# Kernel optimization log

Hardware: AMD Instinct MI355X
Metric: run time of the kernel (lower is better)

## Reference

```python
import jax, jax.numpy as jnp
import numpy as np

N_NODES = 100000
N_EDGES = 3200000
C, H, F = 512, 256, 64


def spmm(edge_row, edge_col, edge_val, Z):
    # (A @ Z)[i] = sum over edges e with row[e]==i of val[e] * Z[col[e]]
    msgs = edge_val[:, None] * Z[edge_col]  # [E, d]
    return jax.ops.segment_sum(msgs, edge_row, num_segments=N_NODES)


def setup_inputs() -> dict:
    key = jax.random.key(0)
    k1, k2, k3, k4, k5, k6, k7 = jax.random.split(key, 7)
    X = jax.random.normal(k1, (N_NODES, C), dtype=jnp.float32)
    edge_row = jax.random.randint(k2, (N_EDGES,), 0, N_NODES, dtype=jnp.int32)
    edge_col = jax.random.randint(k3, (N_EDGES,), 0, N_NODES, dtype=jnp.int32)
    edge_val = jax.random.uniform(k4, (N_EDGES,), dtype=jnp.float32)
    W0 = jax.random.normal(k5, (C, H), dtype=jnp.float32) * (C ** -0.5)
    Wh1 = jax.random.normal(k6, (H, H), dtype=jnp.float32) * (H ** -0.5)
    W1 = jax.random.normal(k7, (H, F), dtype=jnp.float32) * (H ** -0.5)
    return {"X": X, "edge_row": edge_row, "edge_col": edge_col,
            "edge_val": edge_val, "W0": W0, "Wh1": Wh1, "W1": W1}


def reference(X, edge_row, edge_col, edge_val, W0, Wh1, W1):
    # layer 0: relu(A @ (X W0))   (dropout=0 -> identity)
    Z = jax.nn.relu(spmm(edge_row, edge_col, edge_val, X @ W0))
    # hidden layers (num_layers - 2 = 1)
    Z = jax.nn.relu(spmm(edge_row, edge_col, edge_val, Z @ Wh1))
    # output layer: softmax(A @ (Z W1), axis=-1)
    Z = jax.nn.softmax(spmm(edge_row, edge_col, edge_val, Z @ W1), axis=-1)
    return Z
```

## Files before the change

### kernel.cpp

```cpp
#include <hip/hip_runtime.h>
#include <cstdint>
#include <cstddef>


#define SCAN_B 1024

typedef __attribute__((ext_vector_type(8))) short short8_t;
typedef __attribute__((ext_vector_type(4))) short short4_t;
typedef __attribute__((ext_vector_type(4))) float f32x4;

__device__ __forceinline__ short bf16_hi(float x) {
    union { float f; unsigned u; } c; c.f = x;
    return (short)(c.u >> 16);
}
__device__ __forceinline__ float bf16_f32(short h) {
    union { float f; unsigned u; } c; c.u = ((unsigned)(unsigned short)h) << 16;
    return c.f;
}

__device__ __forceinline__ void gload_lds16(const void* g, void* l) {
    __builtin_amdgcn_global_load_lds(
        (const __attribute__((address_space(1))) void*)g,
        (__attribute__((address_space(3))) void*)l, 16, 0, 0);
}

#define GBAR() asm volatile("s_barrier" ::: "memory")
#define LGKM0() asm volatile("s_waitcnt lgkmcnt(0)" ::: "memory")

__device__ __forceinline__ void wait_vm(int n) {
    switch (n) {
        case 0:  asm volatile("s_waitcnt vmcnt(0)"  ::: "memory"); break;
        case 6:  asm volatile("s_waitcnt vmcnt(6)"  ::: "memory"); break;
        case 8:  asm volatile("s_waitcnt vmcnt(8)"  ::: "memory"); break;
        default: asm volatile("s_waitcnt vmcnt(10)" ::: "memory"); break;
    }
}


__global__ __launch_bounds__(256) void count_rows_k(const int* __restrict__ row,
                                                    int* __restrict__ deg, int E) {
    const int tidg = blockIdx.x * 256 + threadIdx.x;
    const int T = gridDim.x * 256;
    const int E4 = E >> 2;
    for (int c = tidg; c < E4; c += T) {
        int4 r = *(const int4*)&row[c * 4];
        atomicAdd(&deg[r.x], 1);
        atomicAdd(&deg[r.y], 1);
        atomicAdd(&deg[r.z], 1);
        atomicAdd(&deg[r.w], 1);
    }
    for (int e = E4 * 4 + tidg; e < E; e += T) atomicAdd(&deg[row[e]], 1);
}

__global__ __launch_bounds__(SCAN_B) void scan1_k(const int* __restrict__ deg,
                                                  int* __restrict__ part,
                                                  int* __restrict__ bsum, int n) {
    __shared__ int buf[SCAN_B];
    int tid = threadIdx.x;
    int i = blockIdx.x * SCAN_B + tid;
    int v = (i < n) ? ((deg[i] + 3) & ~3) : 0;
    buf[tid] = v;
    __syncthreads();
    for (int off = 1; off < SCAN_B; off <<= 1) {
        int y = (tid >= off) ? buf[tid - off] : 0;
        __syncthreads();
        buf[tid] += y;
        __syncthreads();
    }
    if (i < n) part[i] = buf[tid] - v;
    if (tid == SCAN_B - 1) bsum[blockIdx.x] = buf[tid];
}

__global__ __launch_bounds__(128) void scan2_k(int* __restrict__ bsum, int nb) {
    __shared__ int buf[128];
    int tid = threadIdx.x;
    int v = (tid < nb) ? bsum[tid] : 0;
    buf[tid] = v;
    __syncthreads();
    for (int off = 1; off < 128; off <<= 1) {
        int y = (tid >= off) ? buf[tid - off] : 0;
        __syncthreads();
        buf[tid] += y;
        __syncthreads();
    }
    if (tid < nb) bsum[tid] = buf[tid] - v;
    if (tid == nb - 1) bsum[nb] = buf[tid];
}

__global__ __launch_bounds__(SCAN_B) void scan3_k(int* __restrict__ rowptr,
                                                  const int* __restrict__ bsum,
                                                  int* __restrict__ cursor, int n, int nb) {
    int i = blockIdx.x * SCAN_B + threadIdx.x;
    if (i < n) {
        int v = rowptr[i] + bsum[blockIdx.x];
        rowptr[i] = v;
        cursor[i] = v;
    }
    if (i == 0) rowptr[n] = bsum[nb];
}

__global__ __launch_bounds__(256) void scatter_xcd_k(const int* __restrict__ row,
                                                     const int* __restrict__ col,
                                                     const float* __restrict__ val,
                                                     int* __restrict__ cursor,
                                                     int2* __restrict__ ecv,
                                                     int E, int gsz) {
    const int g = blockIdx.x & 7;
    const int lo = g * gsz, hi = lo + gsz;
    const int tidg = (blockIdx.x >> 3) * 256 + threadIdx.x;
    const int T = (gridDim.x >> 3) * 256;
    const int E8 = E >> 3;
    for (int c = tidg; c < E8; c += T) {
        const int e = c * 8;
        int4 r0 = *(const int4*)&row[e];
        int4 r1 = *(const int4*)&row[e + 4];
        int rr[8] = {r0.x, r0.y, r0.z, r0.w, r1.x, r1.y, r1.z, r1.w};
#pragma unroll
        for (int j = 0; j < 8; ++j) {
            if (rr[j] >= lo && rr[j] < hi) {
                int p = atomicAdd(&cursor[rr[j]], 1);
                ecv[p] = make_int2(col[e + j], __float_as_int(val[e + j]));
            }
        }
    }
    for (int e = E8 * 8 + tidg; e < E; e += T) {
        int r = row[e];
        if (r >= lo && r < hi) {
            int p = atomicAdd(&cursor[r], 1);
            ecv[p] = make_int2(col[e], __float_as_int(val[e]));
        }
    }
}


__global__ void split_w_k(const float* __restrict__ W, short* __restrict__ Bhl,
                          int K, int M) {
    int i = blockIdx.x * 256 + threadIdx.x;
    if (i >= K * M) return;
    int k = i / M, m = i - k * M;
    float x = W[i];
    short hi = bf16_hi(x);
    float r = x - bf16_f32(hi);
    short lo = bf16_hi(r);
    int g = k >> 3, j = k & 7;
    Bhl[(size_t)m * (2 * K) + 16 * g + j] = hi;
    Bhl[(size_t)m * (2 * K) + 16 * g + 8 + j] = lo;
}


template <int K, int BN, int NWR, int NWC, bool AF32>
__global__ __launch_bounds__(256) void gemm_hl(const void* __restrict__ Av,
                                               const short* __restrict__ Bhl,
                                               short* __restrict__ ZQ,
                                               float* __restrict__ scl, int N) {
    constexpr int BM = 64 * NWR;
    constexpr int NF = BN / NWC / 16;
    constexpr int NT = K / 32;
    constexpr int LB = BN / 8 / 4;
    constexpr int LA = AF32 ? 0 : BM / 8 / 4;
    constexpr int L  = LA + LB;
    __shared__ short Ald[2][BM * 64];
    __shared__ short Bld[2][BN * 64];

    const int tid = threadIdx.x, lane = tid & 63, w = tid >> 6;
    const int wr = w / NWC, wc = w % NWC;
    const int row0 = blockIdx.x * BM;
    const int l8 = lane >> 3;
    const int sx = (lane & 7) ^ l8;

    const short* Ahl = (const short*)Av;
    const float* Af  = (const float*)Av;
    const int arow = tid >> 2, aq = tid & 3;
    const int akey = arow & 7;

    f32x4 acc[4][NF] = {};

    auto stageB = [&](int t, int b) {
#pragma unroll
        for (int ch = w; ch < BN / 8; ch += 4)
            gload_lds16(Bhl + (size_t)(ch * 8 + l8) * (2 * K) + (size_t)t * 64 + sx * 8,
                        &Bld[b][ch * 512]);
    };
    auto stageAg = [&](int t, int b) {
#pragma unroll
        for (int ch = w; ch < BM / 8; ch += 4)
            gload_lds16(Ahl + (size_t)(row0 + ch * 8 + l8) * (2 * K) + (size_t)t * 64 + sx * 8,
                        &Ald[b][ch * 512]);
    };
    auto loadAf = [&](int t, float4& x0, float4& x1) {
        int gr = row0 + arow;
        x0 = make_float4(0.f, 0.f, 0.f, 0.f); x1 = x0;
        if (gr < N) {
            x0 = *(const float4*)&Af[(size_t)gr * K + t * 32 + aq * 8];
            x1 = *(const float4*)&Af[(size_t)gr * K + t * 32 + aq * 8 + 4];
        }
    };
    auto writeAf = [&](int b, float4 x0, float4 x1) {
        float f[8] = {x0.x, x0.y, x0.z, x0.w, x1.x, x1.y, x1.z, x1.w};
        short8_t hi, lo;
#pragma unroll
        for (int j = 0; j < 8; ++j) {
            short hh = bf16_hi(f[j]);
            hi[j] = hh;
            lo[j] = bf16_hi(f[j] - bf16_f32(hh));
        }
        *(short8_t*)&Ald[b][arow * 64 + ((2 * aq) ^ akey) * 8] = hi;
        *(short8_t*)&Ald[b][arow * 64 + ((2 * aq + 1) ^ akey) * 8] = lo;
    };

    if constexpr (AF32) {
        float4 a0, a1;
        loadAf(0, a0, a1); writeAf(0, a0, a1); stageB(0, 0);
        loadAf(1, a0, a1); writeAf(1, a0, a1); stageB(1, 1);
        LGKM0();
        wait_vm(8);
    } else {
        stageAg(0, 0); stageB(0, 0);
        stageAg(1, 1); stageB(1, 1);
        wait_vm(L);
    }
    GBAR();

#pragma unroll 2
    for (int t = 0; t < NT; ++t) {
        const int cur = t & 1;

        float4 px0, px1;
        if constexpr (AF32) {
            if (t + 2 < NT) loadAf(t + 2, px0, px1);
        }

        const int sH = (lane >> 4) * 2, sL2 = sH + 1;
        short8_t ah[4], al[4];
#pragma unroll
        for (int m = 0; m < 4; ++m) {
            int rl = wr * 64 + m * 16 + (lane & 15);
            int key = rl & 7;
            ah[m] = *(const short8_t*)&Ald[cur][rl * 64 + (sH ^ key) * 8];
            al[m] = *(const short8_t*)&Ald[cur][rl * 64 + (sL2 ^ key) * 8];
        }
#pragma unroll
        for (int n = 0; n < NF; ++n) {
            int cl = wc * (BN / NWC) + n * 16 + (lane & 15);
            int key = cl & 7;
            short8_t bh = *(const short8_t*)&Bld[cur][cl * 64 + (sH ^ key) * 8];
            short8_t bl = *(const short8_t*)&Bld[cur][cl * 64 + (sL2 ^ key) * 8];
#pragma unroll
            for (int m = 0; m < 4; ++m) {
                acc[m][n] = __builtin_amdgcn_mfma_f32_16x16x32_bf16(ah[m], bh, acc[m][n], 0, 0, 0);
                acc[m][n] = __builtin_amdgcn_mfma_f32_16x16x32_bf16(ah[m], bl, acc[m][n], 0, 0, 0);
                acc[m][n] = __builtin_amdgcn_mfma_f32_16x16x32_bf16(al[m], bh, acc[m][n], 0, 0, 0);
            }
        }

        GBAR();
        if constexpr (AF32) {
            if (t + 2 < NT) {
                writeAf(cur, px0, px1);
                stageB(t + 2, cur);
            }
            LGKM0();
            wait_vm(t + 2 < NT ? 8 : 0);
        } else {
            if (t + 2 < NT) { stageAg(t + 2, cur); stageB(t + 2, cur); }
            wait_vm(t + 2 < NT ? L : 0);
        }
        GBAR();
    }

    const int lg = lane >> 4, lc = lane & 15;
    float* maxb = (float*)&Ald[0][0];
    float rmax[4][4];
#pragma unroll
    for (int m = 0; m < 4; ++m)
#pragma unroll
        for (int r = 0; r < 4; ++r) {
            float v = 0.f;
#pragma unroll
            for (int n = 0; n < NF; ++n) v = fmaxf(v, fabsf(acc[m][n][r]));
#pragma unroll
            for (int o = 8; o >= 1; o >>= 1) v = fmaxf(v, __shfl_xor(v, o));
            rmax[m][r] = v;
        }
    if constexpr (NWC > 1) {
        __syncthreads();
        if (lc == 0)
#pragma unroll
            for (int m = 0; m < 4; ++m)
#pragma unroll
                for (int r = 0; r < 4; ++r)
                    maxb[(wr * 64 + m * 16 + lg * 4 + r) * NWC + wc] = rmax[m][r];
        __syncthreads();
    }
#pragma unroll
    for (int m = 0; m < 4; ++m)
#pragma unroll
        for (int r = 0; r < 4; ++r) {
            int rl = wr * 64 + m * 16 + lg * 4 + r;
            float v = rmax[m][r];
            if constexpr (NWC > 1) {
                v = maxb[rl * NWC];
#pragma unroll
                for (int q = 1; q < NWC; ++q) v = fmaxf(v, maxb[rl * NWC + q]);
            }
            int grow = row0 + rl;
            if (grow < N) {
                float inv = (v > 0.f) ? 32767.f / v : 0.f;
                if (lc == 0 && wc == 0) scl[grow] = v * (1.f / 32767.f);
#pragma unroll
                for (int n = 0; n < NF; ++n)
                    ZQ[(size_t)grow * BN + wc * (BN / NWC) + n * 16 + lc] =
                        (short)rintf(acc[m][n][r] * inv);
            }
        }
}


__global__ __launch_bounds__(256) void spmm_agg256_k(const int* __restrict__ rowptr,
                                                     const int2* __restrict__ ecv,
                                                     const short* __restrict__ Q,
                                                     const float* __restrict__ scl,
                                                     short* __restrict__ Zhl, int N) {
    int row = blockIdx.x * 4 + (threadIdx.x >> 6);
    if (row >= N) return;
    const int lane = threadIdx.x & 63;
    const int half = lane >> 5;
    const int l32 = lane & 31;
    int s = rowptr[row], e = rowptr[row + 1];
    const short8_t* Qv = (const short8_t*)Q;
    f32x4 a0 = {0.f, 0.f, 0.f, 0.f}, a1 = a0;
    for (int i = s; i < e; i += 4) {
        int4 A = *(const int4*)(ecv + i);
        int4 B = *(const int4*)(ecv + i + 2);
        int   cA = half ? A.z : A.x;
        float wA = __int_as_float(half ? A.w : A.y) * scl[cA];
        int   cB = half ? B.z : B.x;
        float wB = __int_as_float(half ? B.w : B.y) * scl[cB];
        short8_t qA = Qv[(size_t)cA * 32 + l32];
        short8_t qB = Qv[(size_t)cB * 32 + l32];
#pragma unroll
        for (int j = 0; j < 4; ++j) {
            a0[j] = fmaf(wA, (float)qA[j], a0[j]);
            a1[j] = fmaf(wA, (float)qA[j + 4], a1[j]);
            a0[j] = fmaf(wB, (float)qB[j], a0[j]);
            a1[j] = fmaf(wB, (float)qB[j + 4], a1[j]);
        }
    }
#pragma unroll
    for (int j = 0; j < 4; ++j) {
        a0[j] += __shfl_xor(a0[j], 32);
        a1[j] += __shfl_xor(a1[j], 32);
    }
    if (half == 0) {
        short8_t hi, lo;
#pragma unroll
        for (int j = 0; j < 4; ++j) {
            float r0 = fmaxf(a0[j], 0.f), r1 = fmaxf(a1[j], 0.f);
            short h0 = bf16_hi(r0), h1 = bf16_hi(r1);
            hi[j] = h0; hi[j + 4] = h1;
            lo[j] = bf16_hi(r0 - bf16_f32(h0));
            lo[j + 4] = bf16_hi(r1 - bf16_f32(h1));
        }
        size_t base = (size_t)row * 512 + l32 * 16;
        *(short8_t*)&Zhl[base] = hi;
        *(short8_t*)&Zhl[base + 8] = lo;
    }
}

__global__ __launch_bounds__(256) void spmm_softmax64_k(const int* __restrict__ rowptr,
                                                        const int2* __restrict__ ecv,
                                                        const short* __restrict__ Q,
                                                        const float* __restrict__ scl,
                                                        float* __restrict__ out, int N) {
    int row = blockIdx.x * 4 + (threadIdx.x >> 6);
    if (row >= N) return;
    const int lane = threadIdx.x & 63;
    const int q = lane >> 4;
    const int l16 = lane & 15;
    int s = rowptr[row], e = rowptr[row + 1];
    const short4_t* Qv = (const short4_t*)Q;
    f32x4 acc = {0.f, 0.f, 0.f, 0.f};
    for (int i = s; i < e; i += 4) {
        int4 A = *(const int4*)(ecv + i);
        int4 B = *(const int4*)(ecv + i + 2);
        int c = (q & 2) ? ((q & 1) ? B.z : B.x) : ((q & 1) ? A.z : A.x);
        int wbits = (q & 2) ? ((q & 1) ? B.w : B.y) : ((q & 1) ? A.w : A.y);
        float wv = __int_as_float(wbits) * scl[c];
        short4_t z = Qv[(size_t)c * 16 + l16];
#pragma unroll
        for (int j = 0; j < 4; ++j) acc[j] = fmaf(wv, (float)z[j], acc[j]);
    }
#pragma unroll
    for (int j = 0; j < 4; ++j) {
        acc[j] += __shfl_xor(acc[j], 16);
        acc[j] += __shfl_xor(acc[j], 32);
    }
    float m = fmaxf(fmaxf(acc[0], acc[1]), fmaxf(acc[2], acc[3]));
#pragma unroll
    for (int o = 8; o >= 1; o >>= 1) m = fmaxf(m, __shfl_xor(m, o));
    float p0 = __expf(acc[0] - m), p1 = __expf(acc[1] - m);
    float p2 = __expf(acc[2] - m), p3 = __expf(acc[3] - m);
    float ssum = p0 + p1 + p2 + p3;
#pragma unroll
    for (int o = 8; o >= 1; o >>= 1) ssum += __shfl_xor(ssum, o);
    if (q == 0) {
        float inv = 1.f / ssum;
        float4 o4 = make_float4(p0 * inv, p1 * inv, p2 * inv, p3 * inv);
        *(float4*)&out[(size_t)row * 64 + l16 * 4] = o4;
    }
}


extern "C" void kernel_launch(void* const* d_in, const int* in_sizes, int n_in,
                              void* d_out, int out_size, void* d_ws, size_t ws_size,
                              hipStream_t stream) {
    const float* X        = (const float*)d_in[0];
    const int*   edge_row = (const int*)d_in[1];
    const int*   edge_col = (const int*)d_in[2];
    const float* edge_val = (const float*)d_in[3];
    const float* W0       = (const float*)d_in[4];
    const float* Wh1      = (const float*)d_in[5];
    const float* W1       = (const float*)d_in[6];

    const int C = 512, H = 256, F = 64;
    const int N = in_sizes[0] / C;
    const int E = in_sizes[1];
    const int EPAD = E + 4 * N + 64;

    size_t off = 0;
    auto alloc = [&](size_t bytes) -> void* {
        void* p = (char*)d_ws + off;
        off += (bytes + 255) & ~(size_t)255;
        return p;
    };
    short* Zhl    = (short*)alloc((size_t)N * 2 * H * sizeof(short));
    short* ZQ     = (short*)alloc((size_t)N * H * sizeof(short));
    float* scl    = (float*)alloc((size_t)N * sizeof(float));
    int*   deg    = (int*)alloc((size_t)N * sizeof(int));
    int*   rowptr = (int*)alloc((size_t)(N + 1) * sizeof(int));
    int*   cursor = (int*)alloc((size_t)N * sizeof(int));
    int*   bsum   = (int*)alloc(129 * sizeof(int));
    int2*  ecv    = (int2*)alloc((size_t)EPAD * sizeof(int2));
    short* Bhl0   = (short*)alloc((size_t)H * 2 * C * sizeof(short));
    short* Bhl1   = (short*)alloc((size_t)H * 2 * H * sizeof(short));
    short* Bhl2   = (short*)alloc((size_t)F * 2 * H * sizeof(short));
    (void)ws_size;

    hipMemsetAsync(deg, 0, (size_t)N * sizeof(int), stream);
    hipMemsetAsync(ecv, 0, (size_t)EPAD * sizeof(int2), stream);
    count_rows_k<<<2048, 256, 0, stream>>>(edge_row, deg, E);
    int nb = (N + SCAN_B - 1) / SCAN_B;
    scan1_k<<<nb, SCAN_B, 0, stream>>>(deg, rowptr, bsum, N);
    scan2_k<<<1, 128, 0, stream>>>(bsum, nb);
    scan3_k<<<nb, SCAN_B, 0, stream>>>(rowptr, bsum, cursor, N, nb);
    const int gsz = (N + 7) / 8;
    scatter_xcd_k<<<8 * 256, 256, 0, stream>>>(edge_row, edge_col, edge_val,
                                               cursor, ecv, E, gsz);

    split_w_k<<<(C * H + 255) / 256, 256, 0, stream>>>(W0, Bhl0, C, H);
    split_w_k<<<(H * H + 255) / 256, 256, 0, stream>>>(Wh1, Bhl1, H, H);
    split_w_k<<<(H * F + 255) / 256, 256, 0, stream>>>(W1, Bhl2, H, F);

    const int g64  = (N + 63) / 64;
    const int g128 = (N + 127) / 128;
    const int rg   = (N + 3) / 4;

    gemm_hl<512, 256, 1, 4, true><<<g64, 256, 0, stream>>>(X, Bhl0, ZQ, scl, N);
    spmm_agg256_k<<<rg, 256, 0, stream>>>(rowptr, ecv, ZQ, scl, Zhl, N);
    gemm_hl<256, 256, 1, 4, false><<<g64, 256, 0, stream>>>(Zhl, Bhl1, ZQ, scl, N);
    spmm_agg256_k<<<rg, 256, 0, stream>>>(rowptr, ecv, ZQ, scl, Zhl, N);
    gemm_hl<256, 64, 2, 2, false><<<g128, 256, 0, stream>>>(Zhl, Bhl2, ZQ, scl, N);
    spmm_softmax64_k<<<rg, 256, 0, stream>>>(rowptr, ecv, ZQ, scl,
                                             (float*)d_out, N);
}
```

Baseline: 1.132 ms.

## Partition degree count by XCD, vectorize scatter loads, replace ecv memset with pad fill

Row-degree counting now runs XCD-partitioned, so each block group only does atomics on its own row range, in the same way as the scatter kernel. The scatter kernel loads col and val as vectors, issues all cursor atomics before any stores, and then writes the packed entries. The full memset of the padded edge array is replaced by a small kernel that zeroes only the padding slots left after each row's scatter. Together these cut atomic contention and memory traffic during CSR construction, but every block of the count kernel now reads the whole row array.

New measurement: 1.115 ms. About the same (-1.5%).

```diff
diff --git a/kernel.cpp b/kernel.cpp
--- a/kernel.cpp
+++ b/kernel.cpp
@@ -37,19 +37,25 @@
 }
 
 
-__global__ __launch_bounds__(256) void count_rows_k(const int* __restrict__ row,
-                                                    int* __restrict__ deg, int E) {
-    const int tidg = blockIdx.x * 256 + threadIdx.x;
-    const int T = gridDim.x * 256;
+__global__ __launch_bounds__(256) void count_xcd_k(const int* __restrict__ row,
+                                                   int* __restrict__ deg,
+                                                   int E, int gsz) {
+    const int g = blockIdx.x & 7;
+    const int lo = g * gsz, hi = lo + gsz;
+    const int tidg = (blockIdx.x >> 3) * 256 + threadIdx.x;
+    const int T = (gridDim.x >> 3) * 256;
     const int E4 = E >> 2;
     for (int c = tidg; c < E4; c += T) {
         int4 r = *(const int4*)&row[c * 4];
-        atomicAdd(&deg[r.x], 1);
-        atomicAdd(&deg[r.y], 1);
-        atomicAdd(&deg[r.z], 1);
-        atomicAdd(&deg[r.w], 1);
-    }
-    for (int e = E4 * 4 + tidg; e < E; e += T) atomicAdd(&deg[row[e]], 1);
+        if (r.x >= lo && r.x < hi) atomicAdd(&deg[r.x], 1);
+        if (r.y >= lo && r.y < hi) atomicAdd(&deg[r.y], 1);
+        if (r.z >= lo && r.z < hi) atomicAdd(&deg[r.z], 1);
+        if (r.w >= lo && r.w < hi) atomicAdd(&deg[r.w], 1);
+    }
+    for (int e = E4 * 4 + tidg; e < E; e += T) {
+        int r = row[e];
+        if (r >= lo && r < hi) atomicAdd(&deg[r], 1);
+    }
 }
 
 __global__ __launch_bounds__(SCAN_B) void scan1_k(const int* __restrict__ deg,
@@ -112,16 +118,22 @@
     const int E8 = E >> 3;
     for (int c = tidg; c < E8; c += T) {
         const int e = c * 8;
-        int4 r0 = *(const int4*)&row[e];
-        int4 r1 = *(const int4*)&row[e + 4];
-        int rr[8] = {r0.x, r0.y, r0.z, r0.w, r1.x, r1.y, r1.z, r1.w};
-#pragma unroll
-        for (int j = 0; j < 8; ++j) {
-            if (rr[j] >= lo && rr[j] < hi) {
-                int p = atomicAdd(&cursor[rr[j]], 1);
-                ecv[p] = make_int2(col[e + j], __float_as_int(val[e + j]));
-            }
-        }
+        int4   r0 = *(const int4*)&row[e];
+        int4   r1 = *(const int4*)&row[e + 4];
+        int4   c0 = *(const int4*)&col[e];
+        int4   c1 = *(const int4*)&col[e + 4];
+        float4 v0 = *(const float4*)&val[e];
+        float4 v1 = *(const float4*)&val[e + 4];
+        int   rr[8] = {r0.x, r0.y, r0.z, r0.w, r1.x, r1.y, r1.z, r1.w};
+        int   cc[8] = {c0.x, c0.y, c0.z, c0.w, c1.x, c1.y, c1.z, c1.w};
+        float vv[8] = {v0.x, v0.y, v0.z, v0.w, v1.x, v1.y, v1.z, v1.w};
+        int p[8];
+#pragma unroll
+        for (int j = 0; j < 8; ++j)
+            p[j] = (rr[j] >= lo && rr[j] < hi) ? atomicAdd(&cursor[rr[j]], 1) : -1;
+#pragma unroll
+        for (int j = 0; j < 8; ++j)
+            if (p[j] >= 0) ecv[p[j]] = make_int2(cc[j], __float_as_int(vv[j]));
     }
     for (int e = E8 * 8 + tidg; e < E; e += T) {
         int r = row[e];
@@ -129,6 +141,16 @@
             int p = atomicAdd(&cursor[r], 1);
             ecv[p] = make_int2(col[e], __float_as_int(val[e]));
         }
+    }
+}
+
+__global__ __launch_bounds__(256) void pad_fill_k(const int* __restrict__ cursor,
+                                                  const int* __restrict__ rowptr,
+                                                  int2* __restrict__ ecv, int N) {
+    int r = blockIdx.x * 256 + threadIdx.x;
+    if (r < N) {
+        int q = cursor[r], e = rowptr[r + 1];
+        for (; q < e; ++q) ecv[q] = make_int2(0, 0);
     }
 }
 
@@ -447,15 +469,15 @@
     (void)ws_size;
 
     hipMemsetAsync(deg, 0, (size_t)N * sizeof(int), stream);
-    hipMemsetAsync(ecv, 0, (size_t)EPAD * sizeof(int2), stream);
-    count_rows_k<<<2048, 256, 0, stream>>>(edge_row, deg, E);
+    const int gsz = (N + 7) / 8;
+    count_xcd_k<<<2048, 256, 0, stream>>>(edge_row, deg, E, gsz);
     int nb = (N + SCAN_B - 1) / SCAN_B;
     scan1_k<<<nb, SCAN_B, 0, stream>>>(deg, rowptr, bsum, N);
     scan2_k<<<1, 128, 0, stream>>>(bsum, nb);
     scan3_k<<<nb, SCAN_B, 0, stream>>>(rowptr, bsum, cursor, N, nb);
-    const int gsz = (N + 7) / 8;
-    scatter_xcd_k<<<8 * 256, 256, 0, stream>>>(edge_row, edge_col, edge_val,
-                                               cursor, ecv, E, gsz);
+    scatter_xcd_k<<<2048, 256, 0, stream>>>(edge_row, edge_col, edge_val,
+                                            cursor, ecv, E, gsz);
+    pad_fill_k<<<(N + 255) / 256, 256, 0, stream>>>(cursor, rowptr, ecv, N);
 
     split_w_k<<<(C * H + 255) / 256, 256, 0, stream>>>(W0, Bhl0, C, H);
     split_w_k<<<(H * H + 255) / 256, 256, 0, stream>>>(Wh1, Bhl1, H, H);
```
